# Performance work log

Hardware: AMD Instinct MI355X
Metric: run time of the kernel (lower is better)

## Reference

```python
import jax, jax.numpy as jnp
import numpy as np

GRID = (32, 32, 32)
LOWER = jnp.array([0.0, 0.0, 0.0], jnp.float32)
UPPER = jnp.array([1.0, 1.0, 1.0], jnp.float32)
B = 16
N = 131072
C_IN = 1018          # per-point feature channels; +3 offset +3 xyz = 1024 = nn_channels[0]
D_IN = 1024
C_OUT = 128          # nn_channels[-1]
BN_EPS = 1e-5


def setup_inputs() -> dict:
    key = jax.random.key(0)
    ks = jax.random.split(key, 8)
    W1 = jax.random.normal(ks[5], (D_IN, C_OUT), jnp.float32) / np.sqrt(D_IN).astype(np.float32)
    return {
        "xyz": jax.random.uniform(ks[0], (N, 3), jnp.float32),
        "pred_nocs": jax.random.uniform(ks[1], (N, 3), jnp.float32),
        "per_point_features": jax.random.normal(ks[2], (N, C_IN), jnp.float32),
        "pred_confidence": jax.random.uniform(ks[3], (N, 1), jnp.float32),
        "batch_idx": jnp.sort(jax.random.randint(ks[4], (N,), 0, B, dtype=jnp.int32)),
        "batch_size": B,
        "W1": W1,
        "b1": jnp.zeros((C_OUT,), jnp.float32),
        "g1": jnp.ones((C_OUT,), jnp.float32),
        "be1": jnp.zeros((C_OUT,), jnp.float32),
    }


def _batchnorm_train(x, gamma, beta):
    # torch BatchNorm1d in training mode: biased variance over the batch dim
    m = jnp.mean(x, axis=0)
    v = jnp.mean(jnp.square(x - m), axis=0)
    return (x - m) * jax.lax.rsqrt(v + BN_EPS) * gamma + beta


def reference(xyz, pred_nocs, per_point_features, pred_confidence, batch_idx,
              batch_size, W1, b1, g1, be1):
    gs_f = jnp.array(GRID, jnp.float32)
    gs_i = jnp.array(GRID, jnp.int32)
    # VirtualGrid.get_points_grid_idxs: round to nearest cell, clip into grid
    idx_f = jnp.round((pred_nocs - LOWER) / (UPPER - LOWER) * (gs_f - 1.0))
    idx = jnp.clip(idx_f.astype(jnp.int32), 0, gs_i - 1)  # [N,3]
    # VirtualGrid.idxs_to_points
    grid_pts = idx.astype(jnp.float32) / (gs_f - 1.0) * (UPPER - LOWER) + LOWER
    local_offset = pred_nocs - grid_pts
    feats = jnp.concatenate([per_point_features, local_offset, xyz], axis=-1)  # [N,1024]
    # local_nn: Linear -> ReLU -> PointBatchNorm1D
    h = _batchnorm_train(jax.nn.relu(feats @ W1 + b1), g1, be1)  # [N,128]
    # flatten (b,i,j,k) -> flat grid index
    gx, gy, gz = GRID
    flat = ((batch_idx.astype(jnp.int32) * gx + idx[:, 0]) * gy + idx[:, 1]) * gz + idx[:, 2]
    num_grids = batch_size * gx * gy * gz
    ssum = jax.ops.segment_sum(h, flat, num_segments=num_grids)          # [num_grids,128]
    cnt = jax.ops.segment_sum(jnp.ones((h.shape[0], 1), h.dtype), flat, num_segments=num_grids)
    mean = ssum / jnp.maximum(cnt, 1.0)  # empty cells stay 0 (torch_scatter mean)
    # [num_grids, C] -> [B, gx, gy, gz, C] -> [B, C, gx, gy, gz]
    vol = mean.reshape(batch_size, gx, gy, gz, C_OUT).transpose(0, 4, 1, 2, 3)
    return vol
```

## Files before the change

kernel.cpp:

```cpp
#include <hip/hip_runtime.h>

#define NPTS   131072
#define CIN    1018
#define DIN    1024
#define COUT   128
#define BB     16
#define GDIM   32
#define NCELLS (BB*GDIM*GDIM*GDIM)
#define NREP   8

typedef float          f32x4  __attribute__((ext_vector_type(4)));
typedef __bf16         bf16x8 __attribute__((ext_vector_type(8)));
typedef unsigned short us8    __attribute__((ext_vector_type(8)));

__device__ __forceinline__ unsigned short f2bf(float f) {
    union { float f; unsigned u; } v; v.f = f;
    unsigned r = v.u + 0x7FFFu + ((v.u >> 16) & 1u);
    return (unsigned short)(r >> 16);
}

__device__ __forceinline__ us8 cvt8f(f32x4 lo, f32x4 hi) {
    bf16x8 r;
    r[0] = (__bf16)lo[0]; r[1] = (__bf16)lo[1]; r[2] = (__bf16)lo[2]; r[3] = (__bf16)lo[3];
    r[4] = (__bf16)hi[0]; r[5] = (__bf16)hi[1]; r[6] = (__bf16)hi[2]; r[7] = (__bf16)hi[3];
    return __builtin_bit_cast(us8, r);
}

__device__ __forceinline__ f32x4 MF(us8 a, us8 b, f32x4 c) {
    return __builtin_amdgcn_mfma_f32_16x16x32_bf16(
        __builtin_bit_cast(bf16x8, a), __builtin_bit_cast(bf16x8, b), c, 0, 0, 0);
}

__global__ __launch_bounds__(256) void k_zp(const float* __restrict__ W1,
                                            unsigned short* __restrict__ pw,
                                            int4* __restrict__ zp, int n4) {
    const int t = threadIdx.x;
    if (blockIdx.x < 64) {
        const int g  = blockIdx.x * 256 + t;
        const int l  = g & 63;
        const int cb = (g >> 6) & 7;
        const int ks = g >> 9;
        const int col  = cb * 16 + (l & 15);
        const int krow = ks * 32 + ((l >> 4) * 8);
        unsigned short* dst = pw + (size_t)g * 8;
#pragma unroll
        for (int i = 0; i < 8; ++i) dst[i] = f2bf(W1[(size_t)(krow + i) * COUT + col]);
    } else {
        const int idx = (blockIdx.x - 64) * 256 + t;
        const int4 z = {0, 0, 0, 0};
        for (int i = idx; i < n4; i += 512 * 256) zp[i] = z;
    }
}

__global__ __launch_bounds__(256) void k_prep(const float* __restrict__ xyz,
                                              const float* __restrict__ nocs,
                                              const float* __restrict__ feats,
                                              const int*   __restrict__ bidx,
                                              float* __restrict__ tail,
                                              int*   __restrict__ cellid,
                                              int*   __restrict__ cnt) {
    const int i = blockIdx.x * 256 + threadIdx.x;
    if (i >= NPTS) return;
    int id[3]; float off[3];
#pragma unroll
    for (int d = 0; d < 3; ++d) {
        const float nv = nocs[i * 3 + d];
        int ii = (int)rintf(nv * 31.0f);
        ii = ii < 0 ? 0 : (ii > 31 ? 31 : ii);
        id[d]  = ii;
        off[d] = nv - (float)ii / 31.0f;
    }
    float* tl = tail + (size_t)i * 8;
    tl[0] = feats[(size_t)i * CIN + 1016];
    tl[1] = feats[(size_t)i * CIN + 1017];
    tl[2] = off[0]; tl[3] = off[1]; tl[4] = off[2];
    tl[5] = xyz[i*3+0]; tl[6] = xyz[i*3+1]; tl[7] = xyz[i*3+2];
    const int cell = ((bidx[i] * GDIM + id[0]) * GDIM + id[1]) * GDIM + id[2];
    cellid[i] = cell;
    atomicAdd(&cnt[cell], 1);
}

__global__ __launch_bounds__(256) void k_scanA(const int* __restrict__ cnt,
                                               int* __restrict__ rel,
                                               int* __restrict__ bsum,
                                               int4* __restrict__ cursor) {
    __shared__ int wtot[4], woff[4];
    const int t = threadIdx.x, blk = blockIdx.x;
    const int4 z = {0, 0, 0, 0};
    cursor[blk * 256 + t] = z;
    const int4 c4 = *(const int4*)&cnt[blk * 1024 + t * 4];
    const int s = c4.x + c4.y + c4.z + c4.w;
    int v = s;
    const int lane = t & 63, w = t >> 6;
#pragma unroll
    for (int d = 1; d < 64; d <<= 1) {
        const int u = __shfl_up(v, d);
        if (lane >= d) v += u;
    }
    if (lane == 63) wtot[w] = v;
    __syncthreads();
    if (t == 0) {
        int a = 0;
#pragma unroll
        for (int i = 0; i < 4; ++i) { woff[i] = a; a += wtot[i]; }
        bsum[blk] = a;
    }
    __syncthreads();
    const int excl = woff[w] + v - s;
    int* r = rel + blk * 1024 + t * 4;
    r[0] = excl; r[1] = excl + c4.x;
    r[2] = excl + c4.x + c4.y; r[3] = excl + c4.x + c4.y + c4.z;
}

__global__ __launch_bounds__(256) void k_scanB(const int* __restrict__ bsum,
                                               int* __restrict__ boff) {
    __shared__ int wtot[4], woff[4];
    const int t = threadIdx.x;
    const int2 c2 = *(const int2*)&bsum[t * 2];
    const int s = c2.x + c2.y;
    int v = s;
    const int lane = t & 63, w = t >> 6;
#pragma unroll
    for (int d = 1; d < 64; d <<= 1) {
        const int u = __shfl_up(v, d);
        if (lane >= d) v += u;
    }
    if (lane == 63) wtot[w] = v;
    __syncthreads();
    if (t == 0) {
        int a = 0;
#pragma unroll
        for (int i = 0; i < 4; ++i) { woff[i] = a; a += wtot[i]; }
    }
    __syncthreads();
    const int excl = woff[w] + v - s;
    boff[t * 2] = excl; boff[t * 2 + 1] = excl + c2.x;
}

__global__ __launch_bounds__(256) void k_fill(const int* __restrict__ cellid,
                                              const int* __restrict__ rel,
                                              const int* __restrict__ boff,
                                              int* __restrict__ cursor,
                                              int* __restrict__ dstrow) {
    const int i = blockIdx.x * 256 + threadIdx.x;
    if (i >= NPTS) return;
    const int cell = cellid[i];
    const int slot = atomicAdd(&cursor[cell], 1);
    dstrow[i] = rel[cell] + boff[cell >> 10] + slot;
}


template<int DIRECT>
__global__ void k_gemm(const float* __restrict__ feats,
                       const float* __restrict__ tail,
                       const int*   __restrict__ dstrow,
                       const float* __restrict__ b1,
                       const unsigned short* __restrict__ pw,
                       float* __restrict__ dst,
                       float* __restrict__ gstats) {
    __shared__ float S[3 * 12288];
    const int t = threadIdx.x;
    const int w = t >> 6, l = t & 63;
    const int kgrp = l >> 4, l15 = l & 15;
    const int lb = (blockIdx.x & 7) * ((int)gridDim.x >> 3) + (blockIdx.x >> 3);
    const int row0b = lb * 128;
    const int swz = l15 & 7;
    const int lr = w * 16 + l15;

    f32x4 acc[8];
#pragma unroll
    for (int cb = 0; cb < 8; ++cb) {
#pragma unroll
        for (int d = 0; d < 4; ++d) acc[cb][d] = 0.f;
    }

#define STAGE6(stg, ch) do{                                               \
    float* _base = S + (stg) * 12288;                                     \
    _Pragma("unroll")                                                     \
    for (int _i = 0; _i < 4; ++_i) {            \
        const int _s   = t + _i * 512;                                    \
        const int _row = _s >> 4;                                         \
        const int _c4  = (_s & 15) ^ (_row & 7);                          \
        const int _k   = (ch) * 64 + _c4 * 4;                             \
        const float* _src = (_k < 1016)                                   \
            ? feats + (size_t)(row0b + _row) * CIN + _k                   \
            : tail  + (size_t)(row0b + _row) * 8 + (_k - 1016);           \
        __builtin_amdgcn_global_load_lds(                                 \
            (const __attribute__((address_space(1))) void*)_src,          \
            (__attribute__((address_space(3))) void*)&_base[_s * 4],      \
            16, 0, 0);                                                    \
    }                                                                     \
    _Pragma("unroll")                                                     \
    for (int _i = 0; _i < 2; ++_i) {            \
        const int _s = t + _i * 512;                                      \
        __builtin_amdgcn_global_load_lds(                                 \
            (const __attribute__((address_space(1))) void*)                \
                (pw + (size_t)(ch) * 8192 + (size_t)_s * 8),              \
            (__attribute__((address_space(3))) void*)&_base[8192 + _s*4], \
            16, 0, 0);                                                    \
    }                                                                     \
}while(0)

    STAGE6(0, 0);
    STAGE6(1, 1);
    int cur = 0, nxt2 = 2;
    for (int ch = 0; ch < 16; ++ch) {
        __builtin_amdgcn_sched_barrier(0);
        if (ch == 15) asm volatile("s_waitcnt vmcnt(0)" ::: "memory");
        else          asm volatile("s_waitcnt vmcnt(6)" ::: "memory");
        __builtin_amdgcn_sched_barrier(0);
        __builtin_amdgcn_s_barrier();
        __builtin_amdgcn_sched_barrier(0);
        if (ch + 2 < 16) STAGE6(nxt2, ch + 2);
        const float* bufA = S + cur * 12288;
        const unsigned short* bufB = (const unsigned short*)(bufA + 8192);
#pragma unroll
        for (int ks = 0; ks < 2; ++ks) {
            const int c4a = ks * 8 + kgrp * 2;
            const f32x4 lo = *(const f32x4*)&bufA[lr * 64 + (( c4a      ^ swz) << 2)];
            const f32x4 hi = *(const f32x4*)&bufA[lr * 64 + (((c4a + 1) ^ swz) << 2)];
            const us8 a = cvt8f(lo, hi);
#pragma unroll
            for (int cb = 0; cb < 8; ++cb) {
                const us8 b = *(const us8*)(bufB + (((ks * 8 + cb) * 64) + l) * 8);
                acc[cb] = MF(a, b, acc[cb]);
            }
        }
        __builtin_amdgcn_sched_barrier(0);
        cur  = cur  == 2 ? 0 : cur + 1;
        nxt2 = nxt2 == 2 ? 0 : nxt2 + 1;
    }
#undef STAGE6

    int r0[4];
#pragma unroll
    for (int j = 0; j < 4; ++j)
        r0[j] = dstrow[row0b + w * 16 + kgrp * 4 + j];
    float* grep = gstats + (size_t)((blockIdx.x * 8 + w) & (NREP - 1)) * 256;
#pragma unroll
    for (int cb = 0; cb < 8; ++cb) {
        const int c = cb * 16 + l15;
        const float bias = b1[c];
        float s = 0.f, q = 0.f;
#pragma unroll
        for (int j = 0; j < 4; ++j) {
            float v0 = acc[cb][j] + bias; v0 = v0 > 0.f ? v0 : 0.f;
            if (DIRECT) {
                const int a = r0[j];
                unsafeAtomicAdd(dst + (((size_t)((a >> 15) * COUT + c)) << 15) + (a & 32767), v0);
            } else {
                dst[(size_t)r0[j] * COUT + c] = v0;
            }
            s += v0; q += v0 * v0;
        }
        s += __shfl_xor(s, 16); s += __shfl_xor(s, 32);
        q += __shfl_xor(q, 16); q += __shfl_xor(q, 32);
        if (l < 16) {
            unsafeAtomicAdd(grep + c, s);
            unsafeAtomicAdd(grep + COUT + c, q);
        }
    }
}

__global__ void k_stats(const float* __restrict__ gstats, const float* __restrict__ g1,
                        const float* __restrict__ be1, float* __restrict__ ss) {
    const int c = threadIdx.x;
    float sm = 0.f, sq = 0.f;
#pragma unroll
    for (int r = 0; r < NREP; ++r) {
        sm += gstats[r * 256 + c];
        sq += gstats[r * 256 + COUT + c];
    }
    const float invn = 1.0f / (float)NPTS;
    const float mean = sm * invn;
    float var = sq * invn - mean * mean;
    var = var < 0.f ? 0.f : var;
    const float sc = g1[c] * rsqrtf(var + 1e-5f);
    ss[c] = sc;
    ss[COUT + c] = be1[c] - mean * sc;
}

__global__ __launch_bounds__(256) void k_out(const float* __restrict__ h,
                                             const int* __restrict__ cnt,
                                             const int* __restrict__ rel,
                                             const int* __restrict__ boff,
                                             const float* __restrict__ gstats,
                                             const float* __restrict__ g1,
                                             const float* __restrict__ be1,
                                             float* __restrict__ out) {
    __shared__ float tile[128 * 68];
    __shared__ float linv[64];
    __shared__ float lss[256];
    const int t  = threadIdx.x;
    const int lb = (blockIdx.x & 7) * ((int)gridDim.x >> 3) + (blockIdx.x >> 3);
    const int s0 = lb * 64;
    const int b = s0 >> 15, sp0 = s0 & 32767;
    const int boff0 = boff[s0 >> 10];
    if (t < 64) {
        const int cn = cnt[s0 + t];
        linv[t] = cn > 0 ? 1.0f / (float)cn : 0.f;
    } else if (t >= 128) {
        const int c = t - 128;
        float sm = 0.f, sq = 0.f;
#pragma unroll
        for (int r = 0; r < NREP; ++r) {
            sm += gstats[r * 256 + c];
            sq += gstats[r * 256 + COUT + c];
        }
        const float invn = 1.0f / (float)NPTS;
        const float mean = sm * invn;
        float var = sq * invn - mean * mean;
        var = var < 0.f ? 0.f : var;
        const float sc = g1[c] * rsqrtf(var + 1e-5f);
        lss[c] = sc;
        lss[128 + c] = be1[c] - mean * sc;
    }
    const int q = t & 31, r8 = t >> 5;
#pragma unroll
    for (int rep = 0; rep < 8; ++rep) {
        const int j = r8 + rep * 8;
        const int cj = cnt[s0 + j];
        if (cj > 0) {
            const int st = rel[s0 + j] + boff0;
            f32x4 v; v[0] = v[1] = v[2] = v[3] = 0.f;
            for (int k = 0; k < cj; ++k) {
                const f32x4 hv = *(const f32x4*)&h[(size_t)(st + k) * COUT + q * 4];
                v[0] += hv[0]; v[1] += hv[1]; v[2] += hv[2]; v[3] += hv[3];
            }
#pragma unroll
            for (int d = 0; d < 4; ++d) tile[(q * 4 + d) * 68 + j] = v[d];
        }
    }
    __syncthreads();
    const int qq = t & 15, rr = t >> 4;
#pragma unroll
    for (int p = 0; p < 8; ++p) {
        const int c = p * 16 + rr;
        const float sc = lss[c], sh = lss[128 + c];
        const f32x4 vv = *(const f32x4*)&tile[c * 68 + qq * 4];
        f32x4 o;
#pragma unroll
        for (int d = 0; d < 4; ++d) {
            const float inv = linv[qq * 4 + d];
            o[d] = inv > 0.f ? vv[d] * inv * sc + sh : 0.f;
        }
        *(f32x4*)&out[(((size_t)(b * COUT + c)) << 15) + sp0 + qq * 4] = o;
    }
}

__global__ __launch_bounds__(256) void k_norm_inplace(float* __restrict__ out,
                                                      const int* __restrict__ cnt,
                                                      const float* __restrict__ ss,
                                                      size_t total) {
    const size_t i = ((size_t)blockIdx.x * 256 + threadIdx.x) * 4;
    if (i >= total) return;
    const int c = (int)((i >> 15) & 127);
    const size_t cellb = ((i >> 22) << 15) | (i & 32767);
    f32x4 v = *(f32x4*)&out[i];
    const int4 cn = *(const int4*)&cnt[cellb];
    const float sc = ss[c], sh = ss[COUT + c];
    const int cna[4] = {cn.x, cn.y, cn.z, cn.w};
#pragma unroll
    for (int d = 0; d < 4; ++d)
        v[d] = cna[d] > 0 ? v[d] / (float)cna[d] * sc + sh : 0.f;
    *(f32x4*)&out[i] = v;
}

extern "C" void kernel_launch(void* const* d_in, const int* in_sizes, int n_in,
                              void* d_out, int out_size, void* d_ws, size_t ws_size,
                              hipStream_t stream) {
    const float* xyz   = (const float*)d_in[0];
    const float* nocs  = (const float*)d_in[1];
    const float* feats = (const float*)d_in[2];
    const int*   bidx  = (const int*)d_in[4];
    const float* W1    = (const float*)d_in[6];
    const float* b1    = (const float*)d_in[7];
    const float* g1    = (const float*)d_in[8];
    const float* be1   = (const float*)d_in[9];
    float* out = (float*)d_out;
    float* ws  = (float*)d_ws;

    const size_t HF  = (size_t)NPTS * COUT;
    const size_t STF = NREP * 256;
    const size_t oA_h    = 0;
    const size_t oA_cnt  = HF;
    const size_t oA_st   = oA_cnt + NCELLS;
    const size_t oA_cur  = oA_st + STF;
    const size_t oA_rel  = oA_cur + NCELLS;
    const size_t oA_bof  = oA_rel + NCELLS;
    const size_t oA_dr   = oA_bof + 512;
    const size_t oA_ss   = oA_dr + NPTS;
    const size_t oA_tail = oA_ss + 256;
    const size_t oA_cid  = oA_tail + (size_t)NPTS * 8;
    const size_t oA_pw   = oA_cid + NPTS;
    const size_t needA   = (oA_pw + 65536) * sizeof(float);
    const bool planA = ws_size >= needA;

    const size_t oB_cnt = 0, oB_st = NCELLS, oB_ss = oB_st + STF,
                 oB_tail = oB_ss + 256, oB_cid = oB_tail + (size_t)NPTS * 8,
                 oB_pw = oB_cid + NPTS;

    float* h   = planA ? ws + oA_h : nullptr;
    int*   cnt = (int*)(ws + (planA ? oA_cnt : oB_cnt));
    float* st  = ws + (planA ? oA_st : oB_st);
    int*   cur = planA ? (int*)(ws + oA_cur) : nullptr;
    int*   rel = planA ? (int*)(ws + oA_rel) : nullptr;
    int*   bof = planA ? (int*)(ws + oA_bof) : nullptr;
    int*   dr  = planA ? (int*)(ws + oA_dr) : nullptr;
    float* ssb = ws + (planA ? oA_ss : oB_ss);
    float* tl  = ws + (planA ? oA_tail : oB_tail);
    int*   cid = (int*)(ws + (planA ? oA_cid : oB_cid));
    unsigned short* pw = (unsigned short*)(ws + (planA ? oA_pw : oB_pw));

    k_zp<<<576, 256, 0, stream>>>(W1, pw, (int4*)cnt, (int)((NCELLS + STF) / 4));
    if (!planA) hipMemsetAsync(out, 0, (size_t)out_size * sizeof(float), stream);

    k_prep<<<NPTS / 256, 256, 0, stream>>>(xyz, nocs, feats, bidx, tl, cid, cnt);
    if (planA) {
        k_scanA<<<512, 256, 0, stream>>>(cnt, rel, bof, (int4*)cur);
        k_scanB<<<1, 256, 0, stream>>>(bof, bof);
        k_fill<<<NPTS / 256, 256, 0, stream>>>(cid, rel, bof, cur, dr);
        k_gemm<0><<<NPTS / 128, 512, 0, stream>>>(feats, tl, dr, b1, pw, h, st);
        k_out<<<NCELLS / 64, 256, 0, stream>>>(h, cnt, rel, bof, st, g1, be1, out);
    } else {
        k_gemm<1><<<NPTS / 128, 512, 0, stream>>>(feats, tl, cid, b1, pw, out, st);
        k_stats<<<1, 128, 0, stream>>>(st, g1, be1, ssb);
        const size_t total = (size_t)out_size;
        k_norm_inplace<<<(unsigned)((total + 1023) / 1024), 256, 0, stream>>>(out, cnt, ssb, total);
    }
    (void)in_sizes; (void)n_in; (void)d_in;
}
```

Before: 307.1 us.

## Load GEMM weights directly into registers and shrink GEMM tile to 64 rows

```diff
diff --git a/kernel.cpp b/kernel.cpp
--- a/kernel.cpp
+++ b/kernel.cpp
@@ -150,35 +150,20 @@
 }
 
 
-template<int DIRECT>
-__global__ void k_gemm(const float* __restrict__ feats,
-                       const float* __restrict__ tail,
-                       const int*   __restrict__ dstrow,
-                       const float* __restrict__ b1,
-                       const unsigned short* __restrict__ pw,
-                       float* __restrict__ dst,
-                       float* __restrict__ gstats) {
-    __shared__ float S[3 * 12288];
-    const int t = threadIdx.x;
-    const int w = t >> 6, l = t & 63;
-    const int kgrp = l >> 4, l15 = l & 15;
-    const int lb = (blockIdx.x & 7) * ((int)gridDim.x >> 3) + (blockIdx.x >> 3);
-    const int row0b = lb * 128;
-    const int swz = l15 & 7;
-    const int lr = w * 16 + l15;
-
-    f32x4 acc[8];
-#pragma unroll
-    for (int cb = 0; cb < 8; ++cb) {
-#pragma unroll
-        for (int d = 0; d < 4; ++d) acc[cb][d] = 0.f;
-    }
-
-#define STAGE6(stg, ch) do{                                               \
-    float* _base = S + (stg) * 12288;                                     \
+#define LOADB3(B, ch) do{                                                 \
+    _Pragma("unroll")                                                     \
+    for (int _ks = 0; _ks < 2; ++_ks)                                     \
+        _Pragma("unroll")                                                 \
+        for (int _cb = 0; _cb < 8; ++_cb)                                 \
+            B[_ks][_cb] = *(const us8*)(pw +                              \
+                ((((size_t)(ch)*2 + _ks)*8 + _cb)*64 + l)*8);             \
+}while(0)
+
+#define STAGEA(stg, ch) do{                                               \
+    float* _base = S + (stg) * 4096;                                      \
     _Pragma("unroll")                                                     \
     for (int _i = 0; _i < 4; ++_i) {            \
-        const int _s   = t + _i * 512;                                    \
+        const int _s   = t + _i * 256;                                    \
         const int _row = _s >> 4;                                         \
         const int _c4  = (_s & 15) ^ (_row & 7);                          \
         const int _k   = (ch) * 64 + _c4 * 4;                             \
@@ -190,53 +175,76 @@
             (__attribute__((address_space(3))) void*)&_base[_s * 4],      \
             16, 0, 0);                                                    \
     }                                                                     \
+}while(0)
+
+#define COMPUTE3(stg, B) do{                                              \
+    const float* bufA = S + (stg) * 4096;                                 \
     _Pragma("unroll")                                                     \
-    for (int _i = 0; _i < 2; ++_i) {            \
-        const int _s = t + _i * 512;                                      \
-        __builtin_amdgcn_global_load_lds(                                 \
-            (const __attribute__((address_space(1))) void*)                \
-                (pw + (size_t)(ch) * 8192 + (size_t)_s * 8),              \
-            (__attribute__((address_space(3))) void*)&_base[8192 + _s*4], \
-            16, 0, 0);                                                    \
+    for (int ks = 0; ks < 2; ++ks) {                                      \
+        const int c4a = ks * 8 + kgrp * 2;                                \
+        const f32x4 lo = *(const f32x4*)&bufA[lr * 64 + (( c4a      ^ swz) << 2)]; \
+        const f32x4 hi = *(const f32x4*)&bufA[lr * 64 + (((c4a + 1) ^ swz) << 2)]; \
+        const us8 a = cvt8f(lo, hi);                                      \
+        _Pragma("unroll")                                                 \
+        for (int cb = 0; cb < 8; ++cb) acc[cb] = MF(a, B[ks][cb], acc[cb]); \
     }                                                                     \
 }while(0)
 
-    STAGE6(0, 0);
-    STAGE6(1, 1);
-    int cur = 0, nxt2 = 2;
+template<int DIRECT>
+__global__ __launch_bounds__(256) void k_gemm(const float* __restrict__ feats,
+                       const float* __restrict__ tail,
+                       const int*   __restrict__ dstrow,
+                       const float* __restrict__ b1,
+                       const unsigned short* __restrict__ pw,
+                       float* __restrict__ dst,
+                       float* __restrict__ gstats) {
+    __shared__ float S[3 * 4096];
+    const int t = threadIdx.x;
+    const int w = t >> 6, l = t & 63;
+    const int kgrp = l >> 4, l15 = l & 15;
+    const int lb = (blockIdx.x & 7) * ((int)gridDim.x >> 3) + (blockIdx.x >> 3);
+    const int row0b = lb * 64;
+    const int swz = l15 & 7;
+    const int lr = w * 16 + l15;
+
+    f32x4 acc[8];
+#pragma unroll
+    for (int cb = 0; cb < 8; ++cb) {
+#pragma unroll
+        for (int d = 0; d < 4; ++d) acc[cb][d] = 0.f;
+    }
+    us8 Bs0[2][8], Bs1[2][8];
+
+    STAGEA(0, 0);
+    STAGEA(1, 1);
+    __builtin_amdgcn_sched_barrier(0);
+    LOADB3(Bs0, 0);
+    __builtin_amdgcn_sched_barrier(0);
+
+#pragma unroll
     for (int ch = 0; ch < 16; ++ch) {
+        if (ch + 1 < 16) {
+            if (((ch + 1) & 1) == 0) LOADB3(Bs0, ch + 1);
+            else                     LOADB3(Bs1, ch + 1);
+        }
         __builtin_amdgcn_sched_barrier(0);
-        if (ch == 15) asm volatile("s_waitcnt vmcnt(0)" ::: "memory");
-        else          asm volatile("s_waitcnt vmcnt(6)" ::: "memory");
+        if (ch == 15) asm volatile("s_waitcnt vmcnt(0)"  ::: "memory");
+        else          asm volatile("s_waitcnt vmcnt(36)" ::: "memory");
         __builtin_amdgcn_sched_barrier(0);
         __builtin_amdgcn_s_barrier();
         __builtin_amdgcn_sched_barrier(0);
-        if (ch + 2 < 16) STAGE6(nxt2, ch + 2);
-        const float* bufA = S + cur * 12288;
-        const unsigned short* bufB = (const unsigned short*)(bufA + 8192);
-#pragma unroll
-        for (int ks = 0; ks < 2; ++ks) {
-            const int c4a = ks * 8 + kgrp * 2;
-            const f32x4 lo = *(const f32x4*)&bufA[lr * 64 + (( c4a      ^ swz) << 2)];
-            const f32x4 hi = *(const f32x4*)&bufA[lr * 64 + (((c4a + 1) ^ swz) << 2)];
-            const us8 a = cvt8f(lo, hi);
-#pragma unroll
-            for (int cb = 0; cb < 8; ++cb) {
-                const us8 b = *(const us8*)(bufB + (((ks * 8 + cb) * 64) + l) * 8);
-                acc[cb] = MF(a, b, acc[cb]);
-            }
-        }
+        if (ch + 2 < 16) STAGEA((ch + 2) % 3, ch + 2);
         __builtin_amdgcn_sched_barrier(0);
-        cur  = cur  == 2 ? 0 : cur + 1;
-        nxt2 = nxt2 == 2 ? 0 : nxt2 + 1;
-    }
-#undef STAGE6
+        if ((ch & 1) == 0) COMPUTE3(ch % 3, Bs0);
+        else               COMPUTE3(ch % 3, Bs1);
+        __builtin_amdgcn_sched_barrier(0);
+    }
 
     int r0[4];
 #pragma unroll
     for (int j = 0; j < 4; ++j)
         r0[j] = dstrow[row0b + w * 16 + kgrp * 4 + j];
-    float* grep = gstats + (size_t)((blockIdx.x * 8 + w) & (NREP - 1)) * 256;
+    float* grep = gstats + (size_t)((blockIdx.x * 4 + w) & (NREP - 1)) * 256;
 #pragma unroll
     for (int cb = 0; cb < 8; ++cb) {
         const int c = cb * 16 + l15;
@@ -420,10 +428,10 @@
         k_scanA<<<512, 256, 0, stream>>>(cnt, rel, bof, (int4*)cur);
         k_scanB<<<1, 256, 0, stream>>>(bof, bof);
         k_fill<<<NPTS / 256, 256, 0, stream>>>(cid, rel, bof, cur, dr);
-        k_gemm<0><<<NPTS / 128, 512, 0, stream>>>(feats, tl, dr, b1, pw, h, st);
+        k_gemm<0><<<NPTS / 64, 256, 0, stream>>>(feats, tl, dr, b1, pw, h, st);
         k_out<<<NCELLS / 64, 256, 0, stream>>>(h, cnt, rel, bof, st, g1, be1, out);
     } else {
-        k_gemm<1><<<NPTS / 128, 512, 0, stream>>>(feats, tl, cid, b1, pw, out, st);
+        k_gemm<1><<<NPTS / 64, 256, 0, stream>>>(feats, tl, cid, b1, pw, out, st);
         k_stats<<<1, 128, 0, stream>>>(st, g1, be1, ssb);
         const size_t total = (size_t)out_size;
         k_norm_inplace<<<(unsigned)((total + 1023) / 1024), 256, 0, stream>>>(out, cnt, ssb, total);
```

After: 320.0 us. 1.04x slower.
